# Kernel tuning notes

Hardware: AMD Instinct MI355X
Metric: run time of the kernel (lower is better)

## Reference

```python
import jax, jax.numpy as jnp
import numpy as np

N, B, S, CIN, E, H = 8192, 4, 2816, 64, 128, 8
HD = E // H


def setup_inputs() -> dict:
    key = jax.random.key(0)
    ks = jax.random.split(key, 8)
    b_ids = jnp.sort(jax.random.randint(ks[0], (N,), 0, B))
    other = jax.random.randint(ks[1], (N, 3), 0, 100)
    voxel_coords = jnp.concatenate([b_ids[:, None], other], axis=1).astype(jnp.int32)
    s = 0.02
    return {
        'pillar_features': jax.random.normal(ks[2], (N, CIN), jnp.float32),
        'voxel_coords': voxel_coords,
        'batch_size': B,
        'max_pillars': S,
        'pre_w': jax.random.normal(ks[3], (CIN, E), jnp.float32) * s,
        'pre_b': jnp.zeros((E,), jnp.float32),
        'in_w': jax.random.normal(ks[4], (E, 3 * E), jnp.float32) * s,
        'in_b': jnp.zeros((3 * E,), jnp.float32),
        'out_w': jax.random.normal(ks[5], (E, E), jnp.float32) * s,
        'out_b': jnp.zeros((E,), jnp.float32),
        'ln1_g': jnp.ones((E,), jnp.float32),
        'ln1_b': jnp.zeros((E,), jnp.float32),
        'w1': jax.random.normal(ks[6], (E, 2 * E), jnp.float32) * s,
        'b1': jnp.zeros((2 * E,), jnp.float32),
        'w2': jax.random.normal(ks[7], (2 * E, E), jnp.float32) * s,
        'b2': jnp.zeros((E,), jnp.float32),
        'ln2_g': jnp.ones((E,), jnp.float32),
        'ln2_b': jnp.zeros((E,), jnp.float32),
    }


def _ln(x, g, b):
    m = jnp.mean(x, axis=-1, keepdims=True)
    v = jnp.var(x, axis=-1, keepdims=True)
    return (x - m) / jnp.sqrt(v + 1e-5) * g + b


def reference(pillar_features, voxel_coords, batch_size, max_pillars,
              pre_w, pre_b, in_w, in_b, out_w, out_b,
              ln1_g, ln1_b, w1, b1, w2, b2, ln2_g, ln2_b):
    n = pillar_features.shape[0]
    b_ids = voxel_coords[:, 0].astype(jnp.int32)
    counts = jax.ops.segment_sum(jnp.ones((n,), jnp.int32), b_ids, num_segments=batch_size)
    starts = jnp.concatenate([jnp.zeros((1,), jnp.int32), jnp.cumsum(counts)[:-1]])
    pos = jnp.arange(n, dtype=jnp.int32) - starts[b_ids]  # index within each batch (coords sorted by batch)

    # pack ragged pillars -> padded [B, S, C]
    padded = jnp.zeros((batch_size, max_pillars, pillar_features.shape[-1]),
                       pillar_features.dtype).at[b_ids, pos].set(pillar_features)
    valid = jnp.arange(max_pillars)[None, :] < counts[:, None]  # [B, S], True = real pillar

    x = padded @ pre_w + pre_b  # [B, S, E]

    # multi-head self-attention with key padding mask
    qkv = x @ in_w + in_b
    q, k, v = jnp.split(qkv, 3, axis=-1)
    def heads(t):
        return t.reshape(batch_size, max_pillars, H, HD).transpose(0, 2, 1, 3)
    q, k, v = heads(q), heads(k), heads(v)
    scores = jnp.einsum('bhqd,bhkd->bhqk', q, k) / jnp.sqrt(jnp.float32(HD))
    scores = scores + jnp.where(valid[:, None, None, :], 0.0, -1e9)
    attn = jax.nn.softmax(scores, axis=-1)
    ctx = jnp.einsum('bhqk,bhkd->bhqd', attn, v)
    ctx = ctx.transpose(0, 2, 1, 3).reshape(batch_size, max_pillars, E)
    attn_out = ctx @ out_w + out_b

    x = _ln(x + attn_out, ln1_g, ln1_b)
    ffn = jax.nn.gelu(x @ w1 + b1, approximate=False) @ w2 + b2
    x = _ln(x + ffn, ln2_g, ln2_b)

    # unpack back to ragged [N_total, E]
    return x[b_ids, pos]
```

## Files before the change

kernel.cpp:

```cpp
#include <hip/hip_runtime.h>
#include <hip/hip_bf16.h>
#include <math.h>

#define CIN 64
#define E   128
#define H3  384
#define FF  256
#define NH  8
#define HD  16
#define NBATCH 4

typedef __attribute__((ext_vector_type(8))) short short8;
typedef __attribute__((ext_vector_type(16))) float f32x16;
typedef __attribute__((ext_vector_type(4))) uint uint4v;

static __device__ __forceinline__ ushort f2bf(float f) {
    uint u = __float_as_uint(f);
    return (ushort)((u + 0x7fffu + ((u >> 16) & 1u)) >> 16);
}
static __device__ __forceinline__ uint f2bf2(float lo, float hi) {
    uint r;
    asm("v_cvt_pk_bf16_f32 %0, %1, %2" : "=v"(r) : "v"(lo), "v"(hi));
    return r;
}
static __device__ __forceinline__ void plswap(uint& a, uint& b) {
    auto r = __builtin_amdgcn_permlane32_swap(a, b, false, false);
    a = r[0]; b = r[1];
}
static __device__ __forceinline__ short8 mk8(uint a, uint b, uint c, uint d) {
    uint4v v; v[0] = a; v[1] = b; v[2] = c; v[3] = d;
    return __builtin_bit_cast(short8, v);
}

__global__ void k_bounds(const int* __restrict__ coords, int n, int* __restrict__ starts) {
    int i = blockIdx.x * blockDim.x + threadIdx.x;
    if (i >= n) return;
    int cur = coords[i * 4];
    int prev = (i == 0) ? -1 : coords[(i - 1) * 4];
    for (int bb = prev + 1; bb <= cur; ++bb) starts[bb] = i;
    if (i == n - 1)
        for (int bb = cur + 1; bb <= NBATCH; ++bb) starts[bb] = n;
}

__global__ __launch_bounds__(256) void k_wprep(const float* w0, const float* w1, const float* w2,
                                               const float* w3, const float* w4,
                                               ushort* f0, ushort* f1, ushort* f2,
                                               ushort* f3, ushort* f4) {
    const int Ks[5] = {CIN, E, E, E, FF};
    const int Ms[5] = {E, H3, E, FF, E};
    const int m = blockIdx.y;
    const float* src = m == 0 ? w0 : m == 1 ? w1 : m == 2 ? w2 : m == 3 ? w3 : w4;
    ushort* dst = m == 0 ? f0 : m == 1 ? f1 : m == 2 ? f2 : m == 3 ? f3 : f4;
    const int K = Ks[m], M = Ms[m];
    const int CT = M / 32;
    const int total = (K / 16) * CT * 64;
    const int t = blockIdx.x * 256 + threadIdx.x;
    if (t >= total) return;
    const int lane = t & 63;
    const int ct = (t >> 6) % CT;
    const int kt = (t >> 6) / CT;
    const int col = ct * 32 + (lane & 31);
    const int k0 = kt * 16 + 8 * (lane >> 5);
    const float* sp = src + (size_t)k0 * M + col;
    uint a = f2bf2(sp[0], sp[(size_t)M]);
    uint b = f2bf2(sp[2 * (size_t)M], sp[3 * (size_t)M]);
    uint c = f2bf2(sp[4 * (size_t)M], sp[5 * (size_t)M]);
    uint d = f2bf2(sp[6 * (size_t)M], sp[7 * (size_t)M]);
    *(short8*)(dst + (size_t)t * 8) = mk8(a, b, c, d);
}

__global__ __launch_bounds__(256) void k_preqkv(const float* __restrict__ feat, const ushort* __restrict__ wf0,
        const float* __restrict__ pre_b, const ushort* __restrict__ wf1, const float* __restrict__ in_b,
        float* __restrict__ x, ushort* __restrict__ qh, ushort* __restrict__ kh, ushort* __restrict__ vt2,
        int n, int npk) {
    __shared__ ushort sxb[32][136];
    __shared__ ushort lv[4][32][34];
    const int rt = blockIdx.x;
    const int NT = n >> 6;
    const int tid = threadIdx.x, w = tid >> 6, lane = tid & 63;
    const int l31 = lane & 31, hi = lane >> 5;
    const int row = rt * 32 + l31;
    const int gt = rt >> 1, halfT = rt & 1;
    const float SC = 0.25f * 1.4426950408889634f;
    {
        const uint ONE2 = 0x3F803F80u;
        for (int it = tid; it < 512; it += 256) {
            const int hh = it >> 6, rloc = (it >> 2) & 15, seg = it & 3;
            *(uint4*)(vt2 + ((size_t)(hh * NT + gt) * 32 + 16 + rloc) * 64 + halfT * 32 + seg * 8) =
                make_uint4(ONE2, ONE2, ONE2, ONE2);
        }
    }
    {
        f32x16 acc;
#pragma unroll
        for (int i = 0; i < 16; ++i) acc[i] = 0.f;
#pragma unroll
        for (int kt = 0; kt < 4; ++kt) {
            const float* ap = feat + (size_t)row * CIN + kt * 16 + 8 * hi;
            const float4 a0 = *(const float4*)ap;
            const float4 a1 = *(const float4*)(ap + 4);
            const short8 af = mk8(f2bf2(a0.x, a0.y), f2bf2(a0.z, a0.w),
                                  f2bf2(a1.x, a1.y), f2bf2(a1.z, a1.w));
            const short8 bf = *(const short8*)(wf0 + ((size_t)(kt * 4 + w) * 64 + lane) * 8);
            acc = __builtin_amdgcn_mfma_f32_32x32x16_bf16(af, bf, acc, 0, 0, 0);
        }
        const int col = w * 32 + l31;
        const float bj = pre_b[col];
#pragma unroll
        for (int r = 0; r < 16; ++r) {
            const int rowl = (r & 3) + 8 * (r >> 2) + 4 * hi;
            const float v = acc[r] + bj;
            x[(size_t)(rt * 32 + rowl) * E + col] = v;
            sxb[rowl][col] = f2bf(v);
        }
    }
    __syncthreads();
#pragma unroll
    for (int c = 0; c < 3; ++c) {
        const int ct = w + 4 * c;
        f32x16 acc;
#pragma unroll
        for (int i = 0; i < 16; ++i) acc[i] = 0.f;
#pragma unroll
        for (int kt = 0; kt < 8; ++kt) {
            const short8 af = *(const short8*)(&sxb[l31][kt * 16 + 8 * hi]);
            const short8 bf = *(const short8*)(wf1 + ((size_t)(kt * 12 + ct) * 64 + lane) * 8);
            acc = __builtin_amdgcn_mfma_f32_32x32x16_bf16(af, bf, acc, 0, 0, 0);
        }
        const int colg = ct * 32 + l31;
        const float bj = in_b[colg];
        if (c == 0) {
            const int hh = colg >> 4, d = colg & 15;
#pragma unroll
            for (int r = 0; r < 16; r += 2) {
                const int rowl = (r & 3) + 8 * (r >> 2) + 4 * hi;
                const int grow = rt * 32 + rowl;
                const uint u = f2bf2((acc[r] + bj) * SC, (acc[r + 1] + bj) * SC);
                qh[((size_t)hh * npk + grow) * 16 + d] = (ushort)u;
                qh[((size_t)hh * npk + grow + 1) * 16 + d] = (ushort)(u >> 16);
            }
        } else if (c == 1) {
            const int cg2 = colg - E;
            const int hh = cg2 >> 4, d = cg2 & 15;
#pragma unroll
            for (int r = 0; r < 16; r += 2) {
                const int rowl = (r & 3) + 8 * (r >> 2) + 4 * hi;
                const int grow = rt * 32 + rowl;
                const uint u = f2bf2(acc[r] + bj, acc[r + 1] + bj);
                kh[((size_t)hh * npk + grow) * 16 + d] = (ushort)u;
                kh[((size_t)hh * npk + grow + 1) * 16 + d] = (ushort)(u >> 16);
            }
        } else {
#pragma unroll
            for (int r = 0; r < 16; ++r) {
                const int rowl = (r & 3) + 8 * (r >> 2) + 4 * hi;
                lv[w][l31][rowl] = f2bf(acc[r] + bj);
            }
            const int d = lane >> 1, half = lane & 1;
            const int dg = (ct - 8) * 32 + d;
            const int hh = dg >> 4, dl = dg & 15;
            const short8 v0 = *(const short8*)(&lv[w][d][16 * half]);
            const short8 v1 = *(const short8*)(&lv[w][d][16 * half + 8]);
            ushort* dst = vt2 + ((size_t)(hh * NT + gt) * 32 + dl) * 64 + halfT * 32 + 16 * half;
            *(short8*)dst = v0;
            *(short8*)(dst + 8) = v1;
        }
    }
}

__global__ __launch_bounds__(512) void k_attn12(const ushort* __restrict__ qh, const ushort* __restrict__ kh,
        const ushort* __restrict__ vt2, const int* __restrict__ starts, ushort* __restrict__ ctxb,
        int n, int npk) {
    __shared__ float po[8][32][17];
    const int NT = n >> 6;
    const int bid = blockIdx.x;
    const int h = bid & 7;
    const int bx = bid >> 3;
    const int tid = threadIdx.x, lane = tid & 63, w = tid >> 6;
    int b = -1, bt = 0, s = 0, e = 0, cum = 0;
    for (int bb = 0; bb < NBATCH; ++bb) {
        int sb = starts[bb], eb = starts[bb + 1];
        int t = (eb - (sb & ~31) + 31) >> 5;
        if (b < 0 && bx < cum + t) { b = bb; bt = bx - cum; s = sb; e = eb; }
        cum += t;
    }
    if (b < 0) return;
    const int q0 = (s & ~31) + bt * 32;
    const int l31 = lane & 31, hi = lane >> 5;
    const short8 qf = *(const short8*)(qh + ((size_t)h * npk + q0 + l31) * 16 + 8 * hi);
    const int ks64 = s & ~63;
    const int ntk = (e - ks64 + 63) >> 6;
    const int tw = (ntk + 7) >> 3;
    const int t0 = w * tw, t1 = min(ntk, t0 + tw);

    f32x16 o, z;
#pragma unroll
    for (int i = 0; i < 16; ++i) { o[i] = 0.f; z[i] = 0.f; }

    const ushort* kbase = kh + ((size_t)h * npk + ks64 + l31) * 16 + 8 * hi;
    const ushort* vbase = vt2 + ((size_t)(h * NT + (ks64 >> 6)) * 32 + l31) * 64 + 8 * hi;

    for (int tt = t0; tt < t1; ++tt) {
        const ushort* kp = kbase + (size_t)tt * 1024;
        const short8 ck0 = *(const short8*)kp;
        const short8 ck1 = *(const short8*)(kp + 512);
        const ushort* vt = vbase + (size_t)tt * 2048;
        const short8 vf0 = *(const short8*)(vt);
        const short8 vf1 = *(const short8*)(vt + 16);
        const short8 vf2 = *(const short8*)(vt + 32);
        const short8 vf3 = *(const short8*)(vt + 48);
        f32x16 sf0 = __builtin_amdgcn_mfma_f32_32x32x16_bf16(ck0, qf, z, 0, 0, 0);
        f32x16 sf1 = __builtin_amdgcn_mfma_f32_32x32x16_bf16(ck1, qf, z, 0, 0, 0);
        if (tt == 0 || tt == ntk - 1) {
            const int ktg = ks64 + 64 * tt;
#pragma unroll
            for (int r = 0; r < 16; ++r) {
                const int key = ktg + (r & 3) + 8 * (r >> 2) + 4 * hi;
                if (key < s || key >= e) sf0[r] = -1e30f;
                if (key + 32 < s || key + 32 >= e) sf1[r] = -1e30f;
            }
        }
#pragma unroll
        for (int r = 0; r < 16; ++r) sf0[r] = __builtin_amdgcn_exp2f(sf0[r]);
        {
            uint pA0 = f2bf2(sf0[0], sf0[1]),  pA1 = f2bf2(sf0[2], sf0[3]);
            uint pA2 = f2bf2(sf0[4], sf0[5]),  pA3 = f2bf2(sf0[6], sf0[7]);
            uint pA4 = f2bf2(sf0[8], sf0[9]),  pA5 = f2bf2(sf0[10], sf0[11]);
            uint pA6 = f2bf2(sf0[12], sf0[13]), pA7 = f2bf2(sf0[14], sf0[15]);
            plswap(pA0, pA2); plswap(pA1, pA3);
            plswap(pA4, pA6); plswap(pA5, pA7);
            o = __builtin_amdgcn_mfma_f32_32x32x16_bf16(vf0, mk8(pA0, pA1, pA2, pA3), o, 0, 0, 0);
            o = __builtin_amdgcn_mfma_f32_32x32x16_bf16(vf1, mk8(pA4, pA5, pA6, pA7), o, 0, 0, 0);
        }
#pragma unroll
        for (int r = 0; r < 16; ++r) sf1[r] = __builtin_amdgcn_exp2f(sf1[r]);
        {
            uint pB0 = f2bf2(sf1[0], sf1[1]),  pB1 = f2bf2(sf1[2], sf1[3]);
            uint pB2 = f2bf2(sf1[4], sf1[5]),  pB3 = f2bf2(sf1[6], sf1[7]);
            uint pB4 = f2bf2(sf1[8], sf1[9]),  pB5 = f2bf2(sf1[10], sf1[11]);
            uint pB6 = f2bf2(sf1[12], sf1[13]), pB7 = f2bf2(sf1[14], sf1[15]);
            plswap(pB0, pB2); plswap(pB1, pB3);
            plswap(pB4, pB6); plswap(pB5, pB7);
            o = __builtin_amdgcn_mfma_f32_32x32x16_bf16(vf2, mk8(pB0, pB1, pB2, pB3), o, 0, 0, 0);
            o = __builtin_amdgcn_mfma_f32_32x32x16_bf16(vf3, mk8(pB4, pB5, pB6, pB7), o, 0, 0, 0);
        }
    }
#pragma unroll
    for (int r = 0; r < 8; ++r) {
        const int d = (r & 3) + 8 * (r >> 2) + 4 * hi;
        po[w][l31][d] = o[r];
    }
    if (hi == 0) po[w][l31][16] = o[8];
    __syncthreads();
    if (tid < 256) {
        const int q = tid & 31, d0 = (tid >> 5) * 2;
        const int rowq = q0 + q;
        if (rowq >= s && rowq < e) {
            float L = 0.f, a0 = 0.f, a1 = 0.f;
#pragma unroll
            for (int ww = 0; ww < 8; ++ww) {
                L += po[ww][q][16];
                a0 += po[ww][q][d0];
                a1 += po[ww][q][d0 + 1];
            }
            const float inv = 1.f / L;
            *(uint*)(ctxb + (size_t)rowq * E + h * HD + d0) = f2bf2(a0 * inv, a1 * inv);
        }
    }
}

__global__ __launch_bounds__(256) void k_post(const ushort* __restrict__ ctxb, const ushort* __restrict__ wf2,
        const float* __restrict__ ob, const float* __restrict__ x,
        const float* __restrict__ g1, const float* __restrict__ be1,
        const ushort* __restrict__ wf3, const float* __restrict__ b1,
        const ushort* __restrict__ wf4, const float* __restrict__ b2,
        const float* __restrict__ g2, const float* __restrict__ be2,
        float* __restrict__ out, int n) {
    __shared__ float ly[32][132];
    __shared__ ushort sxb[32][136];
    __shared__ ushort hbt[32][264];
    const int rt = blockIdx.x;
    const int tid = threadIdx.x, w = tid >> 6, lane = tid & 63;
    const int l31 = lane & 31, hi = lane >> 5;
    const int row = rt * 32 + l31;
    {
        f32x16 acc;
#pragma unroll
        for (int i = 0; i < 16; ++i) acc[i] = 0.f;
#pragma unroll
        for (int kt = 0; kt < 8; ++kt) {
            const short8 af = *(const short8*)(ctxb + (size_t)row * E + kt * 16 + 8 * hi);
            const short8 bf = *(const short8*)(wf2 + ((size_t)(kt * 4 + w) * 64 + lane) * 8);
            acc = __builtin_amdgcn_mfma_f32_32x32x16_bf16(af, bf, acc, 0, 0, 0);
        }
        const int col = w * 32 + l31;
        const float bj = ob[col];
#pragma unroll
        for (int r = 0; r < 16; ++r) {
            const int rowl = (r & 3) + 8 * (r >> 2) + 4 * hi;
            ly[rowl][col] = acc[r] + bj + x[(size_t)(rt * 32 + rowl) * E + col];
        }
    }
    __syncthreads();
    {
        const int r = tid >> 3, j = tid & 7;
        float* lrow = ly[r];
        float v[16];
#pragma unroll
        for (int q = 0; q < 4; ++q) {
            const float4 t = *(const float4*)(lrow + 16 * j + 4 * q);
            v[4 * q] = t.x; v[4 * q + 1] = t.y; v[4 * q + 2] = t.z; v[4 * q + 3] = t.w;
        }
        float s = 0.f, ss = 0.f;
#pragma unroll
        for (int i = 0; i < 16; ++i) { s += v[i]; ss += v[i] * v[i]; }
        for (int m = 1; m < 8; m <<= 1) { s += __shfl_xor(s, m); ss += __shfl_xor(ss, m); }
        const float mean = s * (1.f / 128.f);
        const float var = ss * (1.f / 128.f) - mean * mean;
        const float rstd = rsqrtf(var + 1e-5f);
        float zv[16];
#pragma unroll
        for (int q = 0; q < 4; ++q) {
            const float4 gg = *(const float4*)(g1 + 16 * j + 4 * q);
            const float4 bb = *(const float4*)(be1 + 16 * j + 4 * q);
            zv[4 * q]     = (v[4 * q] - mean) * rstd * gg.x + bb.x;
            zv[4 * q + 1] = (v[4 * q + 1] - mean) * rstd * gg.y + bb.y;
            zv[4 * q + 2] = (v[4 * q + 2] - mean) * rstd * gg.z + bb.z;
            zv[4 * q + 3] = (v[4 * q + 3] - mean) * rstd * gg.w + bb.w;
            *(float4*)(lrow + 16 * j + 4 * q) = make_float4(zv[4 * q], zv[4 * q + 1], zv[4 * q + 2], zv[4 * q + 3]);
        }
        *(uint4*)(&sxb[r][16 * j]) =
            make_uint4(f2bf2(zv[0], zv[1]), f2bf2(zv[2], zv[3]), f2bf2(zv[4], zv[5]), f2bf2(zv[6], zv[7]));
        *(uint4*)(&sxb[r][16 * j + 8]) =
            make_uint4(f2bf2(zv[8], zv[9]), f2bf2(zv[10], zv[11]), f2bf2(zv[12], zv[13]), f2bf2(zv[14], zv[15]));
    }
    __syncthreads();
#pragma unroll
    for (int c = 0; c < 2; ++c) {
        const int ct = w + 4 * c;
        f32x16 acc;
#pragma unroll
        for (int i = 0; i < 16; ++i) acc[i] = 0.f;
#pragma unroll
        for (int kt = 0; kt < 8; ++kt) {
            const short8 af = *(const short8*)(&sxb[l31][kt * 16 + 8 * hi]);
            const short8 bf = *(const short8*)(wf3 + ((size_t)(kt * 8 + ct) * 64 + lane) * 8);
            acc = __builtin_amdgcn_mfma_f32_32x32x16_bf16(af, bf, acc, 0, 0, 0);
        }
        const int col = ct * 32 + l31;
        const float bj = b1[col];
#pragma unroll
        for (int r = 0; r < 16; ++r) {
            const int rowl = (r & 3) + 8 * (r >> 2) + 4 * hi;
            const float vv = acc[r] + bj;
            hbt[rowl][col] = f2bf(0.5f * vv * (1.f + erff(vv * 0.7071067811865475f)));
        }
    }
    __syncthreads();
    float res[16];
    {
        f32x16 acc;
#pragma unroll
        for (int i = 0; i < 16; ++i) acc[i] = 0.f;
#pragma unroll
        for (int kt = 0; kt < 16; ++kt) {
            const short8 af = *(const short8*)(&hbt[l31][kt * 16 + 8 * hi]);
            const short8 bf = *(const short8*)(wf4 + ((size_t)(kt * 4 + w) * 64 + lane) * 8);
            acc = __builtin_amdgcn_mfma_f32_32x32x16_bf16(af, bf, acc, 0, 0, 0);
        }
        const int col = w * 32 + l31;
        const float bj = b2[col];
#pragma unroll
        for (int r = 0; r < 16; ++r) {
            const int rowl = (r & 3) + 8 * (r >> 2) + 4 * hi;
            res[r] = acc[r] + bj + ly[rowl][col];
        }
    }
    __syncthreads();
    {
        const int col = w * 32 + l31;
#pragma unroll
        for (int r = 0; r < 16; ++r) {
            const int rowl = (r & 3) + 8 * (r >> 2) + 4 * hi;
            ly[rowl][col] = res[r];
        }
    }
    __syncthreads();
    {
        const int r = tid >> 3, j = tid & 7;
        const float* lrow = ly[r];
        float v[16];
#pragma unroll
        for (int q = 0; q < 4; ++q) {
            const float4 t = *(const float4*)(lrow + 16 * j + 4 * q);
            v[4 * q] = t.x; v[4 * q + 1] = t.y; v[4 * q + 2] = t.z; v[4 * q + 3] = t.w;
        }
        float s = 0.f, ss = 0.f;
#pragma unroll
        for (int i = 0; i < 16; ++i) { s += v[i]; ss += v[i] * v[i]; }
        for (int m = 1; m < 8; m <<= 1) { s += __shfl_xor(s, m); ss += __shfl_xor(ss, m); }
        const float mean = s * (1.f / 128.f);
        const float var = ss * (1.f / 128.f) - mean * mean;
        const float rstd = rsqrtf(var + 1e-5f);
        const int grow = rt * 32 + r;
#pragma unroll
        for (int q = 0; q < 4; ++q) {
            const float4 gg = *(const float4*)(g2 + 16 * j + 4 * q);
            const float4 bb = *(const float4*)(be2 + 16 * j + 4 * q);
            float4 o;
            o.x = (v[4 * q] - mean) * rstd * gg.x + bb.x;
            o.y = (v[4 * q + 1] - mean) * rstd * gg.y + bb.y;
            o.z = (v[4 * q + 2] - mean) * rstd * gg.z + bb.z;
            o.w = (v[4 * q + 3] - mean) * rstd * gg.w + bb.w;
            *(float4*)(out + (size_t)grow * E + 16 * j + 4 * q) = o;
        }
    }
}

extern "C" void kernel_launch(void* const* d_in, const int* in_sizes, int n_in,
                              void* d_out, int out_size, void* d_ws, size_t ws_size,
                              hipStream_t stream) {
    const float* feat   = (const float*)d_in[0];
    const int*   coords = (const int*)d_in[1];
    const float* pre_w  = (const float*)d_in[4];
    const float* pre_b  = (const float*)d_in[5];
    const float* in_w   = (const float*)d_in[6];
    const float* in_b   = (const float*)d_in[7];
    const float* out_w  = (const float*)d_in[8];
    const float* out_b  = (const float*)d_in[9];
    const float* ln1_g  = (const float*)d_in[10];
    const float* ln1_b  = (const float*)d_in[11];
    const float* w1     = (const float*)d_in[12];
    const float* b1     = (const float*)d_in[13];
    const float* w2     = (const float*)d_in[14];
    const float* b2     = (const float*)d_in[15];
    const float* ln2_g  = (const float*)d_in[16];
    const float* ln2_b  = (const float*)d_in[17];
    float* out = (float*)d_out;

    const int n = in_sizes[0] / CIN;
    const int RT = n / 32;
    const int npk = n + 64;
    const int NT = n / 64;

    char* wsb = (char*)d_ws;
    int* starts = (int*)wsb;
    float* x    = (float*)(wsb + 256);
    ushort* qh  = (ushort*)(x + (size_t)n * E);
    ushort* kh  = qh + (size_t)NH * npk * 16;
    ushort* vt2 = kh + (size_t)NH * npk * 16;
    ushort* ctxb = vt2 + (size_t)NH * NT * 32 * 64;
    ushort* wf0 = ctxb + (size_t)n * E;
    ushort* wf1 = wf0 + 4 * 4 * 64 * 8;
    ushort* wf2 = wf1 + 8 * 12 * 64 * 8;
    ushort* wf3 = wf2 + 8 * 4 * 64 * 8;
    ushort* wf4 = wf3 + 8 * 8 * 64 * 8;

    k_bounds<<<dim3((n + 255) / 256), dim3(256), 0, stream>>>(coords, n, starts);
    k_wprep<<<dim3(24, 5), dim3(256), 0, stream>>>(pre_w, in_w, out_w, w1, w2, wf0, wf1, wf2, wf3, wf4);
    k_preqkv<<<dim3(RT), dim3(256), 0, stream>>>(feat, wf0, pre_b, wf1, in_b, x, qh, kh, vt2, n, npk);
    k_attn12<<<dim3((n / 32 + NBATCH) * NH), dim3(512), 0, stream>>>(qh, kh, vt2, starts, ctxb, n, npk);
    k_post<<<dim3(RT), dim3(256), 0, stream>>>(ctxb, wf2, out_b, x, ln1_g, ln1_b,
                                               wf3, b1, wf4, b2, ln2_g, ln2_b, out, n);
}
```

Before: 76.26 us.

## Restructure attention blocks to 4 query tiles x 2 key halves; fuse bounds into wprep

The attention kernel now handles 128 queries per block, with four query tiles each split across two key halves, replacing 32 queries split eight ways over keys. This cuts the number of blocks, shrinks the cross-wave reduction, and reuses each K/V tile load across more queries, at the cost of longer per-wave key loops. The batch-boundary computation is merged into the weight-prep launch as an extra grid row, removing one kernel launch. The query/key padding is widened to n+128 to cover the larger tiles.

New measurement: 85.67 us. +12.3%, slower.

```diff
diff --git a/kernel.cpp b/kernel.cpp
--- a/kernel.cpp
+++ b/kernel.cpp
@@ -32,29 +32,30 @@
     return __builtin_bit_cast(short8, v);
 }
 
-__global__ void k_bounds(const int* __restrict__ coords, int n, int* __restrict__ starts) {
-    int i = blockIdx.x * blockDim.x + threadIdx.x;
-    if (i >= n) return;
-    int cur = coords[i * 4];
-    int prev = (i == 0) ? -1 : coords[(i - 1) * 4];
-    for (int bb = prev + 1; bb <= cur; ++bb) starts[bb] = i;
-    if (i == n - 1)
-        for (int bb = cur + 1; bb <= NBATCH; ++bb) starts[bb] = n;
-}
-
 __global__ __launch_bounds__(256) void k_wprep(const float* w0, const float* w1, const float* w2,
                                                const float* w3, const float* w4,
                                                ushort* f0, ushort* f1, ushort* f2,
-                                               ushort* f3, ushort* f4) {
+                                               ushort* f3, ushort* f4,
+                                               const int* __restrict__ coords, int n,
+                                               int* __restrict__ starts) {
+    const int m = blockIdx.y;
+    const int t = blockIdx.x * 256 + threadIdx.x;
+    if (m == 5) {
+        if (t >= n) return;
+        int cur = coords[t * 4];
+        int prev = (t == 0) ? -1 : coords[(t - 1) * 4];
+        for (int bb = prev + 1; bb <= cur; ++bb) starts[bb] = t;
+        if (t == n - 1)
+            for (int bb = cur + 1; bb <= NBATCH; ++bb) starts[bb] = n;
+        return;
+    }
     const int Ks[5] = {CIN, E, E, E, FF};
     const int Ms[5] = {E, H3, E, FF, E};
-    const int m = blockIdx.y;
     const float* src = m == 0 ? w0 : m == 1 ? w1 : m == 2 ? w2 : m == 3 ? w3 : w4;
     ushort* dst = m == 0 ? f0 : m == 1 ? f1 : m == 2 ? f2 : m == 3 ? f3 : f4;
     const int K = Ks[m], M = Ms[m];
     const int CT = M / 32;
     const int total = (K / 16) * CT * 64;
-    const int t = blockIdx.x * 256 + threadIdx.x;
     if (t >= total) return;
     const int lane = t & 63;
     const int ct = (t >> 6) % CT;
@@ -168,7 +169,7 @@
     }
 }
 
-__global__ __launch_bounds__(512) void k_attn12(const ushort* __restrict__ qh, const ushort* __restrict__ kh,
+__global__ __launch_bounds__(512) void k_attn13(const ushort* __restrict__ qh, const ushort* __restrict__ kh,
         const ushort* __restrict__ vt2, const int* __restrict__ starts, ushort* __restrict__ ctxb,
         int n, int npk) {
     __shared__ float po[8][32][17];
@@ -177,21 +178,23 @@
     const int h = bid & 7;
     const int bx = bid >> 3;
     const int tid = threadIdx.x, lane = tid & 63, w = tid >> 6;
+    const int qt = w & 3, half = w >> 2;
     int b = -1, bt = 0, s = 0, e = 0, cum = 0;
     for (int bb = 0; bb < NBATCH; ++bb) {
         int sb = starts[bb], eb = starts[bb + 1];
-        int t = (eb - (sb & ~31) + 31) >> 5;
+        int t = (eb - (sb & ~31) + 127) >> 7;
         if (b < 0 && bx < cum + t) { b = bb; bt = bx - cum; s = sb; e = eb; }
         cum += t;
     }
     if (b < 0) return;
-    const int q0 = (s & ~31) + bt * 32;
+    const int qbase = (s & ~31) + bt * 128;
+    const int q0 = qbase + qt * 32;
     const int l31 = lane & 31, hi = lane >> 5;
     const short8 qf = *(const short8*)(qh + ((size_t)h * npk + q0 + l31) * 16 + 8 * hi);
     const int ks64 = s & ~63;
     const int ntk = (e - ks64 + 63) >> 6;
-    const int tw = (ntk + 7) >> 3;
-    const int t0 = w * tw, t1 = min(ntk, t0 + tw);
+    const int tw = (ntk + 1) >> 1;
+    const int t0 = half * tw, t1 = min(ntk, t0 + tw);
 
     f32x16 o, z;
 #pragma unroll
@@ -252,20 +255,19 @@
     }
     if (hi == 0) po[w][l31][16] = o[8];
     __syncthreads();
-    if (tid < 256) {
-        const int q = tid & 31, d0 = (tid >> 5) * 2;
-        const int rowq = q0 + q;
-        if (rowq >= s && rowq < e) {
-            float L = 0.f, a0 = 0.f, a1 = 0.f;
-#pragma unroll
-            for (int ww = 0; ww < 8; ++ww) {
-                L += po[ww][q][16];
-                a0 += po[ww][q][d0];
-                a1 += po[ww][q][d0 + 1];
-            }
-            const float inv = 1.f / L;
-            *(uint*)(ctxb + (size_t)rowq * E + h * HD + d0) = f2bf2(a0 * inv, a1 * inv);
-        }
+    const int qt2 = tid >> 7;
+    const int rem = tid & 127;
+    const int q = rem & 31, dp = rem >> 5;
+    const int rowq = qbase + qt2 * 32 + q;
+    if (rowq >= s && rowq < e) {
+        const float L = po[qt2][q][16] + po[4 + qt2][q][16];
+        const float inv = 1.f / L;
+        const float a0 = po[qt2][q][4 * dp]     + po[4 + qt2][q][4 * dp];
+        const float a1 = po[qt2][q][4 * dp + 1] + po[4 + qt2][q][4 * dp + 1];
+        const float a2 = po[qt2][q][4 * dp + 2] + po[4 + qt2][q][4 * dp + 2];
+        const float a3 = po[qt2][q][4 * dp + 3] + po[4 + qt2][q][4 * dp + 3];
+        *(uint2*)(ctxb + (size_t)rowq * E + h * HD + 4 * dp) =
+            make_uint2(f2bf2(a0 * inv, a1 * inv), f2bf2(a2 * inv, a3 * inv));
     }
 }
 
@@ -440,7 +442,7 @@
 
     const int n = in_sizes[0] / CIN;
     const int RT = n / 32;
-    const int npk = n + 64;
+    const int npk = n + 128;
     const int NT = n / 64;
 
     char* wsb = (char*)d_ws;
@@ -456,10 +458,10 @@
     ushort* wf3 = wf2 + 8 * 4 * 64 * 8;
     ushort* wf4 = wf3 + 8 * 8 * 64 * 8;
 
-    k_bounds<<<dim3((n + 255) / 256), dim3(256), 0, stream>>>(coords, n, starts);
-    k_wprep<<<dim3(24, 5), dim3(256), 0, stream>>>(pre_w, in_w, out_w, w1, w2, wf0, wf1, wf2, wf3, wf4);
+    k_wprep<<<dim3(32, 6), dim3(256), 0, stream>>>(pre_w, in_w, out_w, w1, w2,
+                                                   wf0, wf1, wf2, wf3, wf4, coords, n, starts);
     k_preqkv<<<dim3(RT), dim3(256), 0, stream>>>(feat, wf0, pre_b, wf1, in_b, x, qh, kh, vt2, n, npk);
-    k_attn12<<<dim3((n / 32 + NBATCH) * NH), dim3(512), 0, stream>>>(qh, kh, vt2, starts, ctxb, n, npk);
+    k_attn13<<<dim3((n / 128 + NBATCH) * NH), dim3(512), 0, stream>>>(qh, kh, vt2, starts, ctxb, n, npk);
     k_post<<<dim3(RT), dim3(256), 0, stream>>>(ctxb, wf2, out_b, x, ln1_g, ln1_b,
                                                wf3, b1, wf4, b2, ln2_g, ln2_b, out, n);
 }
```

## Software-pipeline QK MFMA in attention, halve waves per block, fuse bounds kernel

Applied to the files above, without the earlier changes.

Folds the batch-bounds computation into the weight-prep kernel as an extra grid row, which removes one kernel launch. The attention kernel drops from 8 to 4 waves per block, so each wave handles twice as many key tiles and the cross-wave reduction shrinks. Inside the key loop, the QK scores for the next tile are computed before the current tile's softmax and PV MFMAs, and s_setprio raises priority around the PV MFMAs. Together these aim to hide MFMA and load latency, at the cost of extra registers, a redundant QK computation on the last iteration, and less parallelism per block.

Measured after the change: 74.61 us. 1.02x faster.

```diff
diff --git a/kernel.cpp b/kernel.cpp
--- a/kernel.cpp
+++ b/kernel.cpp
@@ -32,29 +32,30 @@
     return __builtin_bit_cast(short8, v);
 }
 
-__global__ void k_bounds(const int* __restrict__ coords, int n, int* __restrict__ starts) {
-    int i = blockIdx.x * blockDim.x + threadIdx.x;
-    if (i >= n) return;
-    int cur = coords[i * 4];
-    int prev = (i == 0) ? -1 : coords[(i - 1) * 4];
-    for (int bb = prev + 1; bb <= cur; ++bb) starts[bb] = i;
-    if (i == n - 1)
-        for (int bb = cur + 1; bb <= NBATCH; ++bb) starts[bb] = n;
-}
-
 __global__ __launch_bounds__(256) void k_wprep(const float* w0, const float* w1, const float* w2,
                                                const float* w3, const float* w4,
                                                ushort* f0, ushort* f1, ushort* f2,
-                                               ushort* f3, ushort* f4) {
+                                               ushort* f3, ushort* f4,
+                                               const int* __restrict__ coords, int n,
+                                               int* __restrict__ starts) {
+    const int m = blockIdx.y;
+    const int t = blockIdx.x * 256 + threadIdx.x;
+    if (m == 5) {
+        if (t >= n) return;
+        int cur = coords[t * 4];
+        int prev = (t == 0) ? -1 : coords[(t - 1) * 4];
+        for (int bb = prev + 1; bb <= cur; ++bb) starts[bb] = t;
+        if (t == n - 1)
+            for (int bb = cur + 1; bb <= NBATCH; ++bb) starts[bb] = n;
+        return;
+    }
     const int Ks[5] = {CIN, E, E, E, FF};
     const int Ms[5] = {E, H3, E, FF, E};
-    const int m = blockIdx.y;
     const float* src = m == 0 ? w0 : m == 1 ? w1 : m == 2 ? w2 : m == 3 ? w3 : w4;
     ushort* dst = m == 0 ? f0 : m == 1 ? f1 : m == 2 ? f2 : m == 3 ? f3 : f4;
     const int K = Ks[m], M = Ms[m];
     const int CT = M / 32;
     const int total = (K / 16) * CT * 64;
-    const int t = blockIdx.x * 256 + threadIdx.x;
     if (t >= total) return;
     const int lane = t & 63;
     const int ct = (t >> 6) % CT;
@@ -168,10 +169,10 @@
     }
 }
 
-__global__ __launch_bounds__(512) void k_attn12(const ushort* __restrict__ qh, const ushort* __restrict__ kh,
+__global__ void k_attn14(const ushort* __restrict__ qh, const ushort* __restrict__ kh,
         const ushort* __restrict__ vt2, const int* __restrict__ starts, ushort* __restrict__ ctxb,
         int n, int npk) {
-    __shared__ float po[8][32][17];
+    __shared__ float po[4][32][17];
     const int NT = n >> 6;
     const int bid = blockIdx.x;
     const int h = bid & 7;
@@ -190,7 +191,7 @@
     const short8 qf = *(const short8*)(qh + ((size_t)h * npk + q0 + l31) * 16 + 8 * hi);
     const int ks64 = s & ~63;
     const int ntk = (e - ks64 + 63) >> 6;
-    const int tw = (ntk + 7) >> 3;
+    const int tw = (ntk + 3) >> 2;
     const int t0 = w * tw, t1 = min(ntk, t0 + tw);
 
     f32x16 o, z;
@@ -200,50 +201,64 @@
     const ushort* kbase = kh + ((size_t)h * npk + ks64 + l31) * 16 + 8 * hi;
     const ushort* vbase = vt2 + ((size_t)(h * NT + (ks64 >> 6)) * 32 + l31) * 64 + 8 * hi;
 
-    for (int tt = t0; tt < t1; ++tt) {
-        const ushort* kp = kbase + (size_t)tt * 1024;
+    f32x16 sc0 = z, sc1 = z;
+    if (t0 < t1) {
+        const ushort* kp = kbase + (size_t)t0 * 1024;
         const short8 ck0 = *(const short8*)kp;
         const short8 ck1 = *(const short8*)(kp + 512);
+        sc0 = __builtin_amdgcn_mfma_f32_32x32x16_bf16(ck0, qf, z, 0, 0, 0);
+        sc1 = __builtin_amdgcn_mfma_f32_32x32x16_bf16(ck1, qf, z, 0, 0, 0);
+    }
+    for (int tt = t0; tt < t1; ++tt) {
+        const int ptn = min(tt + 1, t1 - 1);
+        const ushort* kpn = kbase + (size_t)ptn * 1024;
+        const short8 nk0 = *(const short8*)kpn;
+        const short8 nk1 = *(const short8*)(kpn + 512);
+        f32x16 sn0 = __builtin_amdgcn_mfma_f32_32x32x16_bf16(nk0, qf, z, 0, 0, 0);
+        f32x16 sn1 = __builtin_amdgcn_mfma_f32_32x32x16_bf16(nk1, qf, z, 0, 0, 0);
         const ushort* vt = vbase + (size_t)tt * 2048;
         const short8 vf0 = *(const short8*)(vt);
         const short8 vf1 = *(const short8*)(vt + 16);
         const short8 vf2 = *(const short8*)(vt + 32);
         const short8 vf3 = *(const short8*)(vt + 48);
-        f32x16 sf0 = __builtin_amdgcn_mfma_f32_32x32x16_bf16(ck0, qf, z, 0, 0, 0);
-        f32x16 sf1 = __builtin_amdgcn_mfma_f32_32x32x16_bf16(ck1, qf, z, 0, 0, 0);
         if (tt == 0 || tt == ntk - 1) {
             const int ktg = ks64 + 64 * tt;
 #pragma unroll
             for (int r = 0; r < 16; ++r) {
                 const int key = ktg + (r & 3) + 8 * (r >> 2) + 4 * hi;
-                if (key < s || key >= e) sf0[r] = -1e30f;
-                if (key + 32 < s || key + 32 >= e) sf1[r] = -1e30f;
+                if (key < s || key >= e) sc0[r] = -1e30f;
+                if (key + 32 < s || key + 32 >= e) sc1[r] = -1e30f;
             }
         }
 #pragma unroll
-        for (int r = 0; r < 16; ++r) sf0[r] = __builtin_amdgcn_exp2f(sf0[r]);
+        for (int r = 0; r < 16; ++r) sc0[r] = __builtin_amdgcn_exp2f(sc0[r]);
         {
-            uint pA0 = f2bf2(sf0[0], sf0[1]),  pA1 = f2bf2(sf0[2], sf0[3]);
-            uint pA2 = f2bf2(sf0[4], sf0[5]),  pA3 = f2bf2(sf0[6], sf0[7]);
-            uint pA4 = f2bf2(sf0[8], sf0[9]),  pA5 = f2bf2(sf0[10], sf0[11]);
-            uint pA6 = f2bf2(sf0[12], sf0[13]), pA7 = f2bf2(sf0[14], sf0[15]);
+            uint pA0 = f2bf2(sc0[0], sc0[1]),  pA1 = f2bf2(sc0[2], sc0[3]);
+            uint pA2 = f2bf2(sc0[4], sc0[5]),  pA3 = f2bf2(sc0[6], sc0[7]);
+            uint pA4 = f2bf2(sc0[8], sc0[9]),  pA5 = f2bf2(sc0[10], sc0[11]);
+            uint pA6 = f2bf2(sc0[12], sc0[13]), pA7 = f2bf2(sc0[14], sc0[15]);
             plswap(pA0, pA2); plswap(pA1, pA3);
             plswap(pA4, pA6); plswap(pA5, pA7);
+            __builtin_amdgcn_s_setprio(1);
             o = __builtin_amdgcn_mfma_f32_32x32x16_bf16(vf0, mk8(pA0, pA1, pA2, pA3), o, 0, 0, 0);
             o = __builtin_amdgcn_mfma_f32_32x32x16_bf16(vf1, mk8(pA4, pA5, pA6, pA7), o, 0, 0, 0);
-        }
-#pragma unroll
-        for (int r = 0; r < 16; ++r) sf1[r] = __builtin_amdgcn_exp2f(sf1[r]);
+            __builtin_amdgcn_s_setprio(0);
+        }
+#pragma unroll
+        for (int r = 0; r < 16; ++r) sc1[r] = __builtin_amdgcn_exp2f(sc1[r]);
         {
-            uint pB0 = f2bf2(sf1[0], sf1[1]),  pB1 = f2bf2(sf1[2], sf1[3]);
-            uint pB2 = f2bf2(sf1[4], sf1[5]),  pB3 = f2bf2(sf1[6], sf1[7]);
-            uint pB4 = f2bf2(sf1[8], sf1[9]),  pB5 = f2bf2(sf1[10], sf1[11]);
-            uint pB6 = f2bf2(sf1[12], sf1[13]), pB7 = f2bf2(sf1[14], sf1[15]);
+            uint pB0 = f2bf2(sc1[0], sc1[1]),  pB1 = f2bf2(sc1[2], sc1[3]);
+            uint pB2 = f2bf2(sc1[4], sc1[5]),  pB3 = f2bf2(sc1[6], sc1[7]);
+            uint pB4 = f2bf2(sc1[8], sc1[9]),  pB5 = f2bf2(sc1[10], sc1[11]);
+            uint pB6 = f2bf2(sc1[12], sc1[13]), pB7 = f2bf2(sc1[14], sc1[15]);
             plswap(pB0, pB2); plswap(pB1, pB3);
             plswap(pB4, pB6); plswap(pB5, pB7);
+            __builtin_amdgcn_s_setprio(1);
             o = __builtin_amdgcn_mfma_f32_32x32x16_bf16(vf2, mk8(pB0, pB1, pB2, pB3), o, 0, 0, 0);
             o = __builtin_amdgcn_mfma_f32_32x32x16_bf16(vf3, mk8(pB4, pB5, pB6, pB7), o, 0, 0, 0);
-        }
+            __builtin_amdgcn_s_setprio(0);
+        }
+        sc0 = sn0; sc1 = sn1;
     }
 #pragma unroll
     for (int r = 0; r < 8; ++r) {
@@ -252,20 +267,18 @@
     }
     if (hi == 0) po[w][l31][16] = o[8];
     __syncthreads();
-    if (tid < 256) {
-        const int q = tid & 31, d0 = (tid >> 5) * 2;
-        const int rowq = q0 + q;
-        if (rowq >= s && rowq < e) {
-            float L = 0.f, a0 = 0.f, a1 = 0.f;
-#pragma unroll
-            for (int ww = 0; ww < 8; ++ww) {
-                L += po[ww][q][16];
-                a0 += po[ww][q][d0];
-                a1 += po[ww][q][d0 + 1];
-            }
-            const float inv = 1.f / L;
-            *(uint*)(ctxb + (size_t)rowq * E + h * HD + d0) = f2bf2(a0 * inv, a1 * inv);
-        }
+    const int q = tid & 31, d0 = (tid >> 5) * 2;
+    const int rowq = q0 + q;
+    if (rowq >= s && rowq < e) {
+        float L = 0.f, a0 = 0.f, a1 = 0.f;
+#pragma unroll
+        for (int ww = 0; ww < 4; ++ww) {
+            L += po[ww][q][16];
+            a0 += po[ww][q][d0];
+            a1 += po[ww][q][d0 + 1];
+        }
+        const float inv = 1.f / L;
+        *(uint*)(ctxb + (size_t)rowq * E + h * HD + d0) = f2bf2(a0 * inv, a1 * inv);
     }
 }
 
@@ -456,10 +469,10 @@
     ushort* wf3 = wf2 + 8 * 4 * 64 * 8;
     ushort* wf4 = wf3 + 8 * 8 * 64 * 8;
 
-    k_bounds<<<dim3((n + 255) / 256), dim3(256), 0, stream>>>(coords, n, starts);
-    k_wprep<<<dim3(24, 5), dim3(256), 0, stream>>>(pre_w, in_w, out_w, w1, w2, wf0, wf1, wf2, wf3, wf4);
+    k_wprep<<<dim3(32, 6), dim3(256), 0, stream>>>(pre_w, in_w, out_w, w1, w2,
+                                                   wf0, wf1, wf2, wf3, wf4, coords, n, starts);
     k_preqkv<<<dim3(RT), dim3(256), 0, stream>>>(feat, wf0, pre_b, wf1, in_b, x, qh, kh, vt2, n, npk);
-    k_attn12<<<dim3((n / 32 + NBATCH) * NH), dim3(512), 0, stream>>>(qh, kh, vt2, starts, ctxb, n, npk);
+    k_attn14<<<dim3((n / 32 + NBATCH) * NH), dim3(256), 0, stream>>>(qh, kh, vt2, starts, ctxb, n, npk);
     k_post<<<dim3(RT), dim3(256), 0, stream>>>(ctxb, wf2, out_b, x, ln1_g, ln1_b,
                                                wf3, b1, wf4, b2, ln2_g, ln2_b, out, n);
 }
```
